# Kernel optimization log

Hardware: AMD Instinct MI355X
Metric: run time of the kernel (lower is better)

Reference implementation:

```python
import jax, jax.numpy as jnp
import numpy as np

B, T, C, H = 16, 2048, 192, 64

def setup_inputs() -> dict:
    key = jax.random.key(0)
    k1, k2, k3, k4 = jax.random.split(key, 4)
    x = jax.random.normal(k1, (B, T, C), dtype=jnp.float32)
    Wq = jax.random.normal(k2, (C, H), dtype=jnp.float32) * (C ** -0.5)
    Wk = jax.random.normal(k3, (C, H), dtype=jnp.float32) * (C ** -0.5)
    Wv = jax.random.normal(k4, (C, H), dtype=jnp.float32) * (C ** -0.5)
    return {"x": x, "Wq": Wq, "Wk": Wk, "Wv": Wv}

def reference(x, Wq, Wk, Wv):
    # One head of causal self-attention (dropout in eval mode / identity).
    q = x @ Wq                       # [B, T, H]
    k = x @ Wk                       # [B, T, H]
    v = x @ Wv                       # [B, T, H]
    scale = q.shape[-1] ** -0.5
    wei = jnp.einsum('bth,bsh->bts', q, k) * scale   # [B, T, T]
    t = wei.shape[-1]
    causal = jnp.tril(jnp.ones((t, t), dtype=bool))  # tril mask
    wei = jnp.where(causal, wei, -jnp.inf)
    wei = jax.nn.softmax(wei, axis=-1)
    out = jnp.einsum('bts,bsh->bth', wei, v)         # [B, T, H]
    return out
```

## Files before the change

### kernel.cpp

```cpp
#include <hip/hip_runtime.h>

#define B 16
#define T 2048
#define C 192
#define H 64

typedef __bf16 bf16x8 __attribute__((ext_vector_type(8)));
typedef __bf16 bf16x4 __attribute__((ext_vector_type(4)));
typedef float  f32x4  __attribute__((ext_vector_type(4)));

#define MFMA(a, b, c) __builtin_amdgcn_mfma_f32_16x16x32_bf16(a, b, c, 0, 0, 0)

#define SM_BIAS 24.0f

__global__ __launch_bounds__(512) void qkv_mfma_kernel(
    const float* __restrict__ x,
    const float* __restrict__ Wq, const float* __restrict__ Wk,
    const float* __restrict__ Wv,
    __bf16* __restrict__ qb, __bf16* __restrict__ kb, __bf16* __restrict__ vt)
{
    __shared__ __bf16 Ws[192][200];
    __shared__ __bf16 tile[128][72];

    const int tid  = threadIdx.x;
    const int w    = tid >> 6;
    const int lid  = tid & 15;
    const int quad = (tid & 63) >> 4;
    const int m0   = blockIdx.x * 128 + w * 16;

    #pragma unroll
    for (int i = 0; i < 18; i++) {
        const int p = i * 512 + tid;
        const int m = p / 3072;
        const int r = p - m * 3072;
        const int k = r >> 4;
        const int nc4 = (r & 15) << 2;
        const float* W = (m == 0) ? Wq : (m == 1) ? Wk : Wv;
        const float4 v = *(const float4*)(W + k * H + nc4);
        const int n = m * 64 + nc4;
        Ws[n + 0][k] = (__bf16)v.x;
        Ws[n + 1][k] = (__bf16)v.y;
        Ws[n + 2][k] = (__bf16)v.z;
        Ws[n + 3][k] = (__bf16)v.w;
    }

    const float* xrow = x + (size_t)(m0 + lid) * C + quad * 8;
    bf16x8 af[6];
    #pragma unroll
    for (int kc = 0; kc < 6; kc++) {
        const float4 a0 = *(const float4*)(xrow + kc * 32);
        const float4 a1 = *(const float4*)(xrow + kc * 32 + 4);
        af[kc][0] = (__bf16)a0.x; af[kc][1] = (__bf16)a0.y;
        af[kc][2] = (__bf16)a0.z; af[kc][3] = (__bf16)a0.w;
        af[kc][4] = (__bf16)a1.x; af[kc][5] = (__bf16)a1.y;
        af[kc][6] = (__bf16)a1.z; af[kc][7] = (__bf16)a1.w;
    }
    __syncthreads();

    f32x4 acc[12] = {};
    #pragma unroll
    for (int kc = 0; kc < 6; kc++)
        #pragma unroll
        for (int nt = 0; nt < 12; nt++) {
            const bf16x8 bfr =
                *(const bf16x8*)&Ws[nt * 16 + lid][kc * 32 + quad * 8];
            acc[nt] = MFMA(af[kc], bfr, acc[nt]);
        }

    #pragma unroll
    for (int nt = 0; nt < 8; nt++) {
        const int n = nt * 16 + lid;
        __bf16* dst = (n < 64) ? qb : kb;
        const int col = n & 63;
        const float scale = (n < 64) ? 0.1803368801111204f : 1.0f;
        #pragma unroll
        for (int r = 0; r < 4; r++) {
            const int row = m0 + quad * 4 + r;
            dst[(size_t)row * H + col] = (__bf16)(acc[nt][r] * scale);
        }
    }

    #pragma unroll
    for (int nt = 8; nt < 12; nt++) {
        const int col = (nt - 8) * 16 + lid;
        #pragma unroll
        for (int r = 0; r < 4; r++)
            tile[w * 16 + quad * 4 + r][col] = (__bf16)(acc[nt][r]);
    }
    __syncthreads();

    const int bb = blockIdx.x >> 4;
    const int t0 = (blockIdx.x & 15) << 7;
    #pragma unroll
    for (int it = 0; it < 2; ++it) {
        const int q   = it * 512 + tid;
        const int h   = q >> 4;
        const int tl0 = (q & 15) * 8;
        bf16x8 d;
        #pragma unroll
        for (int j = 0; j < 8; j++) d[j] = tile[tl0 + j][h];
        *(bf16x8*)(vt + ((size_t)(bb * H + h)) * T + t0 + tl0) = d;
    }
}

__global__ __launch_bounds__(512, 2) void attn_kernel(
    const __bf16* __restrict__ qb,
    const __bf16* __restrict__ kb,
    const __bf16* __restrict__ vt,
    float* __restrict__ out)
{
    __shared__ __bf16 Kb[2][2][64][72];
    __shared__ __bf16 Vb[2][2][64][68];

    const int tid  = threadIdx.x;
    const int wv   = tid >> 6;
    const int grp  = wv >> 2;
    const int w    = wv & 3;
    const int lid  = tid & 15;
    const int quad = (tid & 63) >> 4;

    const int b   = blockIdx.x & 15;
    const int pr  = blockIdx.x >> 4;
    const int qtH = 31 - pr, qtL = pr;
    const int nchH = qtH + 1;
    const int ntot = 33;
    const size_t bbase = (size_t)b * T;

    const int qH = (qtH << 6) + w * 16;
    const int qL = (qtL << 6) + w * 16;

    const __bf16* qrH = qb + (bbase + qH + lid) * H + quad * 8;
    const bf16x8 qfH0 = *(const bf16x8*)(qrH);
    const bf16x8 qfH1 = *(const bf16x8*)(qrH + 32);
    const __bf16* qrL = qb + (bbase + qL + lid) * H + quad * 8;
    const bf16x8 qfL0 = *(const bf16x8*)(qrL);
    const bf16x8 qfL1 = *(const bf16x8*)(qrL + 32);

    const __bf16* kgb = kb + bbase * H;
    const __bf16* vgb = vt + (size_t)b * H * T;

    const int ra = tid >> 3, ca = (tid & 7) * 8;

    auto keyof = [&](int i) {
        if (i > ntot - 1) i = ntot - 1;
        return (i < nchH ? i : i - nchH) << 6;
    };

    bf16x8 kr[2], vr2[2];
    auto prefetch = [&](int s) {
        #pragma unroll
        for (int g = 0; g < 2; g++) {
            const int key0 = keyof(2 * s + g);
            kr[g]  = *(const bf16x8*)(kgb + (size_t)(key0 + ra) * H + ca);
            vr2[g] = *(const bf16x8*)(vgb + (size_t)ra * T + key0 + ca);
        }
    };

    f32x4 OH[4] = {}, OL[4] = {};
    float lsH = 0.f, lsL = 0.f;

    auto doChunk = [&](f32x4 (&O)[4], float& ls, bf16x8 cq0, bf16x8 cq1,
                       int cqw, int key0, int cur) {
        const __bf16 (*Kc)[72] = Kb[cur][grp];
        const __bf16 (*Vc)[68] = Vb[cur][grp];
        bf16x8 kf[8];
        #pragma unroll
        for (int j = 0; j < 4; j++) {
            kf[2*j]   = *(const bf16x8*)&Kc[j * 16 + lid][quad * 8];
            kf[2*j+1] = *(const bf16x8*)&Kc[j * 16 + lid][32 + quad * 8];
        }
        bf16x8 bv0[4], bv1[4];
        #pragma unroll
        for (int ht = 0; ht < 4; ht++) {
            const __bf16* vr_ = &Vc[ht * 16 + lid][quad * 4];
            ((bf16x4*)&bv0[ht])[0] = *(const bf16x4*)(vr_);
            ((bf16x4*)&bv0[ht])[1] = *(const bf16x4*)(vr_ + 16);
            ((bf16x4*)&bv1[ht])[0] = *(const bf16x4*)(vr_ + 32);
            ((bf16x4*)&bv1[ht])[1] = *(const bf16x4*)(vr_ + 48);
        }
        bf16x8 af0, af1;
        const bool boundary = (key0 + 63 > cqw);
        #pragma unroll
        for (int j = 0; j < 4; j++) {
            f32x4 sS = {-SM_BIAS, -SM_BIAS, -SM_BIAS, -SM_BIAS};
            sS = MFMA(kf[2*j], cq0, sS);
            sS = MFMA(kf[2*j+1], cq1, sS);
            if (boundary) {
                #pragma unroll
                for (int r = 0; r < 4; r++)
                    if (key0 + j * 16 + quad * 4 + r > cqw + lid) sS[r] = -1e30f;
            }
            #pragma unroll
            for (int r = 0; r < 4; r++) {
                const float p = __builtin_amdgcn_exp2f(sS[r]);
                ls += p;
                if      (j == 0) af0[r]     = (__bf16)p;
                else if (j == 1) af0[4 + r] = (__bf16)p;
                else if (j == 2) af1[r]     = (__bf16)p;
                else             af1[4 + r] = (__bf16)p;
            }
        }
        #pragma unroll
        for (int ht = 0; ht < 4; ht++) {
            O[ht] = MFMA(af0, bv0[ht], O[ht]);
            O[ht] = MFMA(af1, bv1[ht], O[ht]);
        }
    };

    prefetch(0);
    int cur = 0;
    for (int s = 0; s < 17; s++) {
        *(bf16x8*)&Kb[cur][0][ra][ca] = kr[0];
        *(bf16x8*)&Kb[cur][1][ra][ca] = kr[1];
        *(bf16x8*)&Vb[cur][0][ra][ca] = vr2[0];
        *(bf16x8*)&Vb[cur][1][ra][ca] = vr2[1];
        __syncthreads();
        if (s + 1 < 17) prefetch(s + 1);

        const int i = 2 * s + grp;
        if (i < ntot) {
            const bool heavy = (i < nchH);
            const int key0 = (heavy ? i : i - nchH) << 6;
            if (heavy) doChunk(OH, lsH, qfH0, qfH1, qH, key0, cur);
            else       doChunk(OL, lsL, qfL0, qfL1, qL, key0, cur);
        }
        cur ^= 1;
    }

    __syncthreads();
    float* sO = (float*)&Kb[0][0][0][0];
    float* sL = (float*)&Vb[0][0][0][0];

    float lh = lsH; lh += __shfl_xor(lh, 16, 64); lh += __shfl_xor(lh, 32, 64);
    float ll = lsL; ll += __shfl_xor(ll, 16, 64); ll += __shfl_xor(ll, 32, 64);

    if (grp == 1) {
        #pragma unroll
        for (int ht = 0; ht < 4; ht++)
            #pragma unroll
            for (int r = 0; r < 4; r++) {
                sO[((0 * 4 + w) * 16 + quad * 4 + r) * 64 + ht * 16 + lid] = OH[ht][r];
                sO[((1 * 4 + w) * 16 + quad * 4 + r) * 64 + ht * 16 + lid] = OL[ht][r];
            }
        if ((tid & 63) < 16) {
            sL[(0 * 4 + w) * 16 + lid] = lh;
            sL[(1 * 4 + w) * 16 + lid] = ll;
        }
    }
    __syncthreads();
    if (grp == 0) {
        lh += sL[(0 * 4 + w) * 16 + lid];
        ll += sL[(1 * 4 + w) * 16 + lid];
        #pragma unroll
        for (int ht = 0; ht < 4; ht++)
            #pragma unroll
            for (int r = 0; r < 4; r++) {
                const float LrH = __shfl(lh, quad * 4 + r, 16);
                const float vH = OH[ht][r]
                    + sO[((0 * 4 + w) * 16 + quad * 4 + r) * 64 + ht * 16 + lid];
                out[(bbase + qH + quad * 4 + r) * H + ht * 16 + lid] = vH / LrH;

                const float LrL = __shfl(ll, quad * 4 + r, 16);
                const float vL = OL[ht][r]
                    + sO[((1 * 4 + w) * 16 + quad * 4 + r) * 64 + ht * 16 + lid];
                out[(bbase + qL + quad * 4 + r) * H + ht * 16 + lid] = vL / LrL;
            }
    }
}

extern "C" void kernel_launch(void* const* d_in, const int* in_sizes, int n_in,
                              void* d_out, int out_size, void* d_ws, size_t ws_size,
                              hipStream_t stream)
{
    const float* x  = (const float*)d_in[0];
    const float* Wq = (const float*)d_in[1];
    const float* Wk = (const float*)d_in[2];
    const float* Wv = (const float*)d_in[3];

    const size_t BTH = (size_t)B * T * H;
    __bf16* qbuf = (__bf16*)d_ws;
    __bf16* kbuf = qbuf + BTH;
    __bf16* vtb  = kbuf + BTH;
    float* outp = (float*)d_out;

    qkv_mfma_kernel<<<B * T / 128, 512, 0, stream>>>(x, Wq, Wk, Wv,
                                                     qbuf, kbuf, vtb);
    attn_kernel<<<B * T / 128, 512, 0, stream>>>(qbuf, kbuf, vtb, outp);
}
```

Before: 105.2 us.

## Load K/V directly from global in attention, split QKV projection across more waves

The attention kernel drops the shared-memory double-buffered K/V staging and block-wide barriers. Each 4-wave group now handles one query tile alone, loading K fragments straight from global memory with register double-buffering and V fragments per chunk. This removes the cross-group LDS reduction at the end. The QKV projection kernel doubles its block to 1024 threads, with each half computing 6 of the 12 output tiles, to cut per-wave accumulator pressure. The cost is redundant global/L2 traffic for K/V across waves, which loses the reuse the shared tiles gave, plus possible occupancy limits from the 1024-thread launch bounds.

```diff
diff --git a/kernel.cpp b/kernel.cpp
--- a/kernel.cpp
+++ b/kernel.cpp
@@ -13,7 +13,7 @@
 
 #define SM_BIAS 24.0f
 
-__global__ __launch_bounds__(512) void qkv_mfma_kernel(
+__global__ __launch_bounds__(1024, 4) void qkv_mfma_kernel(
     const float* __restrict__ x,
     const float* __restrict__ Wq, const float* __restrict__ Wk,
     const float* __restrict__ Wv,
@@ -23,14 +23,16 @@
     __shared__ __bf16 tile[128][72];
 
     const int tid  = threadIdx.x;
-    const int w    = tid >> 6;
+    const int wv   = tid >> 6;
+    const int w8   = wv & 7;
+    const int ng   = wv >> 3;
     const int lid  = tid & 15;
     const int quad = (tid & 63) >> 4;
-    const int m0   = blockIdx.x * 128 + w * 16;
-
-    #pragma unroll
-    for (int i = 0; i < 18; i++) {
-        const int p = i * 512 + tid;
+    const int m0   = blockIdx.x * 128 + w8 * 16;
+
+    #pragma unroll
+    for (int i = 0; i < 9; i++) {
+        const int p = i * 1024 + tid;
         const int m = p / 3072;
         const int r = p - m * 3072;
         const int k = r >> 4;
@@ -57,43 +59,43 @@
     }
     __syncthreads();
 
-    f32x4 acc[12] = {};
+    f32x4 acc[6] = {};
     #pragma unroll
     for (int kc = 0; kc < 6; kc++)
         #pragma unroll
-        for (int nt = 0; nt < 12; nt++) {
+        for (int nt = 0; nt < 6; nt++) {
+            const int ntg = ng * 6 + nt;
             const bf16x8 bfr =
-                *(const bf16x8*)&Ws[nt * 16 + lid][kc * 32 + quad * 8];
+                *(const bf16x8*)&Ws[ntg * 16 + lid][kc * 32 + quad * 8];
             acc[nt] = MFMA(af[kc], bfr, acc[nt]);
         }
 
     #pragma unroll
-    for (int nt = 0; nt < 8; nt++) {
-        const int n = nt * 16 + lid;
-        __bf16* dst = (n < 64) ? qb : kb;
-        const int col = n & 63;
-        const float scale = (n < 64) ? 0.1803368801111204f : 1.0f;
-        #pragma unroll
-        for (int r = 0; r < 4; r++) {
-            const int row = m0 + quad * 4 + r;
-            dst[(size_t)row * H + col] = (__bf16)(acc[nt][r] * scale);
-        }
-    }
-
-    #pragma unroll
-    for (int nt = 8; nt < 12; nt++) {
-        const int col = (nt - 8) * 16 + lid;
-        #pragma unroll
-        for (int r = 0; r < 4; r++)
-            tile[w * 16 + quad * 4 + r][col] = (__bf16)(acc[nt][r]);
+    for (int nt = 0; nt < 6; nt++) {
+        const int ntg = ng * 6 + nt;
+        const int n = ntg * 16 + lid;
+        if (ntg < 8) {
+            __bf16* dst = (n < 64) ? qb : kb;
+            const int col = n & 63;
+            const float scale = (n < 64) ? 0.1803368801111204f : 1.0f;
+            #pragma unroll
+            for (int r = 0; r < 4; r++) {
+                const int row = m0 + quad * 4 + r;
+                dst[(size_t)row * H + col] = (__bf16)(acc[nt][r] * scale);
+            }
+        } else {
+            const int col = n - 128;
+            #pragma unroll
+            for (int r = 0; r < 4; r++)
+                tile[w8 * 16 + quad * 4 + r][col] = (__bf16)(acc[nt][r]);
+        }
     }
     __syncthreads();
 
     const int bb = blockIdx.x >> 4;
     const int t0 = (blockIdx.x & 15) << 7;
-    #pragma unroll
-    for (int it = 0; it < 2; ++it) {
-        const int q   = it * 512 + tid;
+    {
+        const int q   = tid;
         const int h   = q >> 4;
         const int tl0 = (q & 15) * 8;
         bf16x8 d;
@@ -109,9 +111,6 @@
     const __bf16* __restrict__ vt,
     float* __restrict__ out)
 {
-    __shared__ __bf16 Kb[2][2][64][72];
-    __shared__ __bf16 Vb[2][2][64][68];
-
     const int tid  = threadIdx.x;
     const int wv   = tid >> 6;
     const int grp  = wv >> 2;
@@ -121,74 +120,61 @@
 
     const int b   = blockIdx.x & 15;
     const int pr  = blockIdx.x >> 4;
-    const int qtH = 31 - pr, qtL = pr;
-    const int nchH = qtH + 1;
-    const int ntot = 33;
+    const int qt  = grp ? pr : (31 - pr);
+    const int nch = qt + 1;
     const size_t bbase = (size_t)b * T;
-
-    const int qH = (qtH << 6) + w * 16;
-    const int qL = (qtL << 6) + w * 16;
-
-    const __bf16* qrH = qb + (bbase + qH + lid) * H + quad * 8;
-    const bf16x8 qfH0 = *(const bf16x8*)(qrH);
-    const bf16x8 qfH1 = *(const bf16x8*)(qrH + 32);
-    const __bf16* qrL = qb + (bbase + qL + lid) * H + quad * 8;
-    const bf16x8 qfL0 = *(const bf16x8*)(qrL);
-    const bf16x8 qfL1 = *(const bf16x8*)(qrL + 32);
+    const int qX  = (qt << 6) + w * 16;
+
+    const __bf16* qr = qb + (bbase + qX + lid) * H + quad * 8;
+    const bf16x8 qf0 = *(const bf16x8*)(qr);
+    const bf16x8 qf1 = *(const bf16x8*)(qr + 32);
 
     const __bf16* kgb = kb + bbase * H;
     const __bf16* vgb = vt + (size_t)b * H * T;
 
-    const int ra = tid >> 3, ca = (tid & 7) * 8;
-
-    auto keyof = [&](int i) {
-        if (i > ntot - 1) i = ntot - 1;
-        return (i < nchH ? i : i - nchH) << 6;
+    f32x4 O[4] = {};
+    float ls = 0.f;
+
+    bf16x8 kfA[8], kfB[8];
+
+    auto loadK = [&](bf16x8 (&kf)[8], int key0) {
+        #pragma unroll
+        for (int j = 0; j < 4; j++) {
+            const __bf16* kp =
+                kgb + (size_t)(key0 + j * 16 + lid) * H + quad * 8;
+            kf[2 * j]     = *(const bf16x8*)(kp);
+            kf[2 * j + 1] = *(const bf16x8*)(kp + 32);
+        }
     };
 
-    bf16x8 kr[2], vr2[2];
-    auto prefetch = [&](int s) {
-        #pragma unroll
-        for (int g = 0; g < 2; g++) {
-            const int key0 = keyof(2 * s + g);
-            kr[g]  = *(const bf16x8*)(kgb + (size_t)(key0 + ra) * H + ca);
-            vr2[g] = *(const bf16x8*)(vgb + (size_t)ra * T + key0 + ca);
-        }
-    };
-
-    f32x4 OH[4] = {}, OL[4] = {};
-    float lsH = 0.f, lsL = 0.f;
-
-    auto doChunk = [&](f32x4 (&O)[4], float& ls, bf16x8 cq0, bf16x8 cq1,
-                       int cqw, int key0, int cur) {
-        const __bf16 (*Kc)[72] = Kb[cur][grp];
-        const __bf16 (*Vc)[68] = Vb[cur][grp];
-        bf16x8 kf[8];
-        #pragma unroll
-        for (int j = 0; j < 4; j++) {
-            kf[2*j]   = *(const bf16x8*)&Kc[j * 16 + lid][quad * 8];
-            kf[2*j+1] = *(const bf16x8*)&Kc[j * 16 + lid][32 + quad * 8];
-        }
+    auto chunk = [&](bf16x8 (&kf)[8], bf16x8 (&kfn)[8], int i) {
+        if (i >= nch) return;
+        const int key0 = i << 6;
+
         bf16x8 bv0[4], bv1[4];
         #pragma unroll
         for (int ht = 0; ht < 4; ht++) {
-            const __bf16* vr_ = &Vc[ht * 16 + lid][quad * 4];
-            ((bf16x4*)&bv0[ht])[0] = *(const bf16x4*)(vr_);
-            ((bf16x4*)&bv0[ht])[1] = *(const bf16x4*)(vr_ + 16);
-            ((bf16x4*)&bv1[ht])[0] = *(const bf16x4*)(vr_ + 32);
-            ((bf16x4*)&bv1[ht])[1] = *(const bf16x4*)(vr_ + 48);
-        }
+            const __bf16* vp =
+                vgb + (size_t)(ht * 16 + lid) * T + key0 + quad * 4;
+            ((bf16x4*)&bv0[ht])[0] = *(const bf16x4*)(vp);
+            ((bf16x4*)&bv0[ht])[1] = *(const bf16x4*)(vp + 16);
+            ((bf16x4*)&bv1[ht])[0] = *(const bf16x4*)(vp + 32);
+            ((bf16x4*)&bv1[ht])[1] = *(const bf16x4*)(vp + 48);
+        }
+        if (i + 1 < nch) loadK(kfn, (i + 1) << 6);
+
+        const bool boundary = (key0 + 63 > qX);
         bf16x8 af0, af1;
-        const bool boundary = (key0 + 63 > cqw);
         #pragma unroll
         for (int j = 0; j < 4; j++) {
             f32x4 sS = {-SM_BIAS, -SM_BIAS, -SM_BIAS, -SM_BIAS};
-            sS = MFMA(kf[2*j], cq0, sS);
-            sS = MFMA(kf[2*j+1], cq1, sS);
+            sS = MFMA(kf[2 * j], qf0, sS);
+            sS = MFMA(kf[2 * j + 1], qf1, sS);
             if (boundary) {
                 #pragma unroll
                 for (int r = 0; r < 4; r++)
-                    if (key0 + j * 16 + quad * 4 + r > cqw + lid) sS[r] = -1e30f;
+                    if (key0 + j * 16 + quad * 4 + r > qX + lid)
+                        sS[r] = -1e30f;
             }
             #pragma unroll
             for (int r = 0; r < 4; r++) {
@@ -207,65 +193,23 @@
         }
     };
 
-    prefetch(0);
-    int cur = 0;
-    for (int s = 0; s < 17; s++) {
-        *(bf16x8*)&Kb[cur][0][ra][ca] = kr[0];
-        *(bf16x8*)&Kb[cur][1][ra][ca] = kr[1];
-        *(bf16x8*)&Vb[cur][0][ra][ca] = vr2[0];
-        *(bf16x8*)&Vb[cur][1][ra][ca] = vr2[1];
-        __syncthreads();
-        if (s + 1 < 17) prefetch(s + 1);
-
-        const int i = 2 * s + grp;
-        if (i < ntot) {
-            const bool heavy = (i < nchH);
-            const int key0 = (heavy ? i : i - nchH) << 6;
-            if (heavy) doChunk(OH, lsH, qfH0, qfH1, qH, key0, cur);
-            else       doChunk(OL, lsL, qfL0, qfL1, qL, key0, cur);
-        }
-        cur ^= 1;
-    }
-
-    __syncthreads();
-    float* sO = (float*)&Kb[0][0][0][0];
-    float* sL = (float*)&Vb[0][0][0][0];
-
-    float lh = lsH; lh += __shfl_xor(lh, 16, 64); lh += __shfl_xor(lh, 32, 64);
-    float ll = lsL; ll += __shfl_xor(ll, 16, 64); ll += __shfl_xor(ll, 32, 64);
-
-    if (grp == 1) {
-        #pragma unroll
-        for (int ht = 0; ht < 4; ht++)
-            #pragma unroll
-            for (int r = 0; r < 4; r++) {
-                sO[((0 * 4 + w) * 16 + quad * 4 + r) * 64 + ht * 16 + lid] = OH[ht][r];
-                sO[((1 * 4 + w) * 16 + quad * 4 + r) * 64 + ht * 16 + lid] = OL[ht][r];
-            }
-        if ((tid & 63) < 16) {
-            sL[(0 * 4 + w) * 16 + lid] = lh;
-            sL[(1 * 4 + w) * 16 + lid] = ll;
-        }
-    }
-    __syncthreads();
-    if (grp == 0) {
-        lh += sL[(0 * 4 + w) * 16 + lid];
-        ll += sL[(1 * 4 + w) * 16 + lid];
-        #pragma unroll
-        for (int ht = 0; ht < 4; ht++)
-            #pragma unroll
-            for (int r = 0; r < 4; r++) {
-                const float LrH = __shfl(lh, quad * 4 + r, 16);
-                const float vH = OH[ht][r]
-                    + sO[((0 * 4 + w) * 16 + quad * 4 + r) * 64 + ht * 16 + lid];
-                out[(bbase + qH + quad * 4 + r) * H + ht * 16 + lid] = vH / LrH;
-
-                const float LrL = __shfl(ll, quad * 4 + r, 16);
-                const float vL = OL[ht][r]
-                    + sO[((1 * 4 + w) * 16 + quad * 4 + r) * 64 + ht * 16 + lid];
-                out[(bbase + qL + quad * 4 + r) * H + ht * 16 + lid] = vL / LrL;
-            }
-    }
+    loadK(kfA, 0);
+    for (int i = 0; i < nch; i += 2) {
+        chunk(kfA, kfB, i);
+        chunk(kfB, kfA, i + 1);
+    }
+
+    float l = ls;
+    l += __shfl_xor(l, 16, 64);
+    l += __shfl_xor(l, 32, 64);
+    #pragma unroll
+    for (int ht = 0; ht < 4; ht++)
+        #pragma unroll
+        for (int r = 0; r < 4; r++) {
+            const float Lr = __shfl(l, quad * 4 + r, 16);
+            out[(bbase + qX + quad * 4 + r) * H + ht * 16 + lid] =
+                O[ht][r] / Lr;
+        }
 }
 
 extern "C" void kernel_launch(void* const* d_in, const int* in_sizes, int n_in,
@@ -283,7 +227,7 @@
     __bf16* vtb  = kbuf + BTH;
     float* outp = (float*)d_out;
 
-    qkv_mfma_kernel<<<B * T / 128, 512, 0, stream>>>(x, Wq, Wk, Wv,
-                                                     qbuf, kbuf, vtb);
+    qkv_mfma_kernel<<<B * T / 128, 1024, 0, stream>>>(x, Wq, Wk, Wv,
+                                                      qbuf, kbuf, vtb);
     attn_kernel<<<B * T / 128, 512, 0, stream>>>(qbuf, kbuf, vtb, outp);
 }
```

After: 173.3 us. 64.8% more time.

## Split paired heavy/light query tiles into separate blocks with doubled grid

Applied to the files above, without the earlier changes.

Each attention block used to process a heavy and a light 64-row query tile together, always running 17 steps. Now each block handles a single query tile, running a variable number of steps that depends on its causal extent, and the grid is doubled to 512 blocks. Heavy tiles are scheduled first (the first half of the grid) to help load balance. Launch bounds are raised to 4 blocks per CU to allow more occupancy from fewer live registers. The cost is that balanced pairing within a block is lost, so the outcome depends on the hardware block scheduler, and each block re-reads K/V on its own.

```diff
diff --git a/kernel.cpp b/kernel.cpp
--- a/kernel.cpp
+++ b/kernel.cpp
@@ -103,7 +103,7 @@
     }
 }
 
-__global__ __launch_bounds__(512, 2) void attn_kernel(
+__global__ __launch_bounds__(512, 4) void attn_kernel(
     const __bf16* __restrict__ qb,
     const __bf16* __restrict__ kb,
     const __bf16* __restrict__ vt,
@@ -119,22 +119,20 @@
     const int lid  = tid & 15;
     const int quad = (tid & 63) >> 4;
 
-    const int b   = blockIdx.x & 15;
-    const int pr  = blockIdx.x >> 4;
-    const int qtH = 31 - pr, qtL = pr;
-    const int nchH = qtH + 1;
-    const int ntot = 33;
+    const int half = blockIdx.x >> 8;
+    const int rem  = blockIdx.x & 255;
+    const int b    = rem & 15;
+    const int pr   = rem >> 4;
+    const int qt   = half ? pr : (31 - pr);
+    const int nch  = qt + 1;
+    const int nsteps = (nch + 1) >> 1;
     const size_t bbase = (size_t)b * T;
 
-    const int qH = (qtH << 6) + w * 16;
-    const int qL = (qtL << 6) + w * 16;
-
-    const __bf16* qrH = qb + (bbase + qH + lid) * H + quad * 8;
-    const bf16x8 qfH0 = *(const bf16x8*)(qrH);
-    const bf16x8 qfH1 = *(const bf16x8*)(qrH + 32);
-    const __bf16* qrL = qb + (bbase + qL + lid) * H + quad * 8;
-    const bf16x8 qfL0 = *(const bf16x8*)(qrL);
-    const bf16x8 qfL1 = *(const bf16x8*)(qrL + 32);
+    const int qX = (qt << 6) + w * 16;
+
+    const __bf16* qr = qb + (bbase + qX + lid) * H + quad * 8;
+    const bf16x8 qf0 = *(const bf16x8*)(qr);
+    const bf16x8 qf1 = *(const bf16x8*)(qr + 32);
 
     const __bf16* kgb = kb + bbase * H;
     const __bf16* vgb = vt + (size_t)b * H * T;
@@ -142,8 +140,8 @@
     const int ra = tid >> 3, ca = (tid & 7) * 8;
 
     auto keyof = [&](int i) {
-        if (i > ntot - 1) i = ntot - 1;
-        return (i < nchH ? i : i - nchH) << 6;
+        if (i > nch - 1) i = nch - 1;
+        return i << 6;
     };
 
     bf16x8 kr[2], vr2[2];
@@ -156,11 +154,10 @@
         }
     };
 
-    f32x4 OH[4] = {}, OL[4] = {};
-    float lsH = 0.f, lsL = 0.f;
-
-    auto doChunk = [&](f32x4 (&O)[4], float& ls, bf16x8 cq0, bf16x8 cq1,
-                       int cqw, int key0, int cur) {
+    f32x4 O[4] = {};
+    float ls = 0.f;
+
+    auto doChunk = [&](int key0, int cur) {
         const __bf16 (*Kc)[72] = Kb[cur][grp];
         const __bf16 (*Vc)[68] = Vb[cur][grp];
         bf16x8 kf[8];
@@ -179,16 +176,16 @@
             ((bf16x4*)&bv1[ht])[1] = *(const bf16x4*)(vr_ + 48);
         }
         bf16x8 af0, af1;
-        const bool boundary = (key0 + 63 > cqw);
+        const bool boundary = (key0 + 63 > qX);
         #pragma unroll
         for (int j = 0; j < 4; j++) {
             f32x4 sS = {-SM_BIAS, -SM_BIAS, -SM_BIAS, -SM_BIAS};
-            sS = MFMA(kf[2*j], cq0, sS);
-            sS = MFMA(kf[2*j+1], cq1, sS);
+            sS = MFMA(kf[2*j], qf0, sS);
+            sS = MFMA(kf[2*j+1], qf1, sS);
             if (boundary) {
                 #pragma unroll
                 for (int r = 0; r < 4; r++)
-                    if (key0 + j * 16 + quad * 4 + r > cqw + lid) sS[r] = -1e30f;
+                    if (key0 + j * 16 + quad * 4 + r > qX + lid) sS[r] = -1e30f;
             }
             #pragma unroll
             for (int r = 0; r < 4; r++) {
@@ -209,21 +206,16 @@
 
     prefetch(0);
     int cur = 0;
-    for (int s = 0; s < 17; s++) {
+    for (int s = 0; s < nsteps; s++) {
         *(bf16x8*)&Kb[cur][0][ra][ca] = kr[0];
         *(bf16x8*)&Kb[cur][1][ra][ca] = kr[1];
         *(bf16x8*)&Vb[cur][0][ra][ca] = vr2[0];
         *(bf16x8*)&Vb[cur][1][ra][ca] = vr2[1];
         __syncthreads();
-        if (s + 1 < 17) prefetch(s + 1);
+        if (s + 1 < nsteps) prefetch(s + 1);
 
         const int i = 2 * s + grp;
-        if (i < ntot) {
-            const bool heavy = (i < nchH);
-            const int key0 = (heavy ? i : i - nchH) << 6;
-            if (heavy) doChunk(OH, lsH, qfH0, qfH1, qH, key0, cur);
-            else       doChunk(OL, lsL, qfL0, qfL1, qL, key0, cur);
-        }
+        if (i < nch) doChunk(i << 6, cur);
         cur ^= 1;
     }
 
@@ -231,39 +223,29 @@
     float* sO = (float*)&Kb[0][0][0][0];
     float* sL = (float*)&Vb[0][0][0][0];
 
-    float lh = lsH; lh += __shfl_xor(lh, 16, 64); lh += __shfl_xor(lh, 32, 64);
-    float ll = lsL; ll += __shfl_xor(ll, 16, 64); ll += __shfl_xor(ll, 32, 64);
+    float l = ls;
+    l += __shfl_xor(l, 16, 64);
+    l += __shfl_xor(l, 32, 64);
 
     if (grp == 1) {
+        #pragma unroll
+        for (int ht = 0; ht < 4; ht++)
+            #pragma unroll
+            for (int r = 0; r < 4; r++)
+                sO[(w * 16 + quad * 4 + r) * 64 + ht * 16 + lid] = O[ht][r];
+        if ((tid & 63) < 16) sL[w * 16 + lid] = l;
+    }
+    __syncthreads();
+    if (grp == 0) {
+        l += sL[w * 16 + lid];
         #pragma unroll
         for (int ht = 0; ht < 4; ht++)
             #pragma unroll
             for (int r = 0; r < 4; r++) {
-                sO[((0 * 4 + w) * 16 + quad * 4 + r) * 64 + ht * 16 + lid] = OH[ht][r];
-                sO[((1 * 4 + w) * 16 + quad * 4 + r) * 64 + ht * 16 + lid] = OL[ht][r];
-            }
-        if ((tid & 63) < 16) {
-            sL[(0 * 4 + w) * 16 + lid] = lh;
-            sL[(1 * 4 + w) * 16 + lid] = ll;
-        }
-    }
-    __syncthreads();
-    if (grp == 0) {
-        lh += sL[(0 * 4 + w) * 16 + lid];
-        ll += sL[(1 * 4 + w) * 16 + lid];
-        #pragma unroll
-        for (int ht = 0; ht < 4; ht++)
-            #pragma unroll
-            for (int r = 0; r < 4; r++) {
-                const float LrH = __shfl(lh, quad * 4 + r, 16);
-                const float vH = OH[ht][r]
-                    + sO[((0 * 4 + w) * 16 + quad * 4 + r) * 64 + ht * 16 + lid];
-                out[(bbase + qH + quad * 4 + r) * H + ht * 16 + lid] = vH / LrH;
-
-                const float LrL = __shfl(ll, quad * 4 + r, 16);
-                const float vL = OL[ht][r]
-                    + sO[((1 * 4 + w) * 16 + quad * 4 + r) * 64 + ht * 16 + lid];
-                out[(bbase + qL + quad * 4 + r) * H + ht * 16 + lid] = vL / LrL;
+                const float Lr = __shfl(l, quad * 4 + r, 16);
+                const float v = O[ht][r]
+                    + sO[(w * 16 + quad * 4 + r) * 64 + ht * 16 + lid];
+                out[(bbase + qX + quad * 4 + r) * H + ht * 16 + lid] = v / Lr;
             }
     }
 }
@@ -285,5 +267,5 @@
 
     qkv_mfma_kernel<<<B * T / 128, 512, 0, stream>>>(x, Wq, Wk, Wv,
                                                      qbuf, kbuf, vtb);
-    attn_kernel<<<B * T / 128, 512, 0, stream>>>(qbuf, kbuf, vtb, outp);
+    attn_kernel<<<B * T / 128 * 2, 512, 0, stream>>>(qbuf, kbuf, vtb, outp);
 }
```

After: 101.6 us. -3.4%, faster.

## Fuse QKV projection and attention into one cooperative kernel with grid sync

Applied to the files above, without the earlier changes.

Replaces the two-kernel QKV+attention pipeline with a small weight pre-transpose kernel plus a single cooperative kernel. Each block projects exactly the query rows it later attends over, synchronises the whole grid, then runs the unchanged attention loop. Weights are pre-packed in MFMA fragment order so each block loads them with plain vector copies instead of a scattered transpose into shared memory. This saves one kernel launch gap and the per-block weight transpose, but adds an extra small launch and a grid-wide barrier, and needs all 256 blocks to be co-resident.

```diff
diff --git a/kernel.cpp b/kernel.cpp
--- a/kernel.cpp
+++ b/kernel.cpp
@@ -1,4 +1,7 @@
 #include <hip/hip_runtime.h>
+#include <hip/hip_cooperative_groups.h>
+
+namespace cg = cooperative_groups;
 
 #define B 16
 #define T 2048
@@ -13,258 +16,272 @@
 
 #define SM_BIAS 24.0f
 
-__global__ __launch_bounds__(512) void qkv_mfma_kernel(
+__global__ __launch_bounds__(512) void wtrans_kernel(
+    const float* __restrict__ Wq, const float* __restrict__ Wk,
+    const float* __restrict__ Wv, __bf16* __restrict__ Wf)
+{
+    const int idx  = blockIdx.x * 512 + threadIdx.x;
+    const int ntg  = idx / 384;
+    const int rem  = idx - ntg * 384;
+    const int kc   = rem >> 6;
+    const int lane = rem & 63;
+    const float* Wm = (ntg < 4) ? Wq : (ntg < 8) ? Wk : Wv;
+    const int nl = ((ntg & 3) << 4) + (lane & 15);
+    const int k0 = kc * 32 + (lane >> 4) * 8;
+    bf16x8 d;
+    #pragma unroll
+    for (int j = 0; j < 8; j++) d[j] = (__bf16)Wm[(k0 + j) * H + nl];
+    *(bf16x8*)(Wf + (size_t)idx * 8) = d;
+}
+
+__global__ __launch_bounds__(512) void fused_kernel(
     const float* __restrict__ x,
-    const float* __restrict__ Wq, const float* __restrict__ Wk,
-    const float* __restrict__ Wv,
-    __bf16* __restrict__ qb, __bf16* __restrict__ kb, __bf16* __restrict__ vt)
+    const __bf16* __restrict__ Wf,
+    __bf16* __restrict__ qb, __bf16* __restrict__ kb, __bf16* __restrict__ vt,
+    float* __restrict__ out)
 {
-    __shared__ __bf16 Ws[192][200];
-    __shared__ __bf16 tile[128][72];
+    __shared__ __bf16 smem[46080];
 
     const int tid  = threadIdx.x;
-    const int w    = tid >> 6;
     const int lid  = tid & 15;
     const int quad = (tid & 63) >> 4;
-    const int m0   = blockIdx.x * 128 + w * 16;
-
-    #pragma unroll
-    for (int i = 0; i < 18; i++) {
-        const int p = i * 512 + tid;
-        const int m = p / 3072;
-        const int r = p - m * 3072;
-        const int k = r >> 4;
-        const int nc4 = (r & 15) << 2;
-        const float* W = (m == 0) ? Wq : (m == 1) ? Wk : Wv;
-        const float4 v = *(const float4*)(W + k * H + nc4);
-        const int n = m * 64 + nc4;
-        Ws[n + 0][k] = (__bf16)v.x;
-        Ws[n + 1][k] = (__bf16)v.y;
-        Ws[n + 2][k] = (__bf16)v.z;
-        Ws[n + 3][k] = (__bf16)v.w;
-    }
-
-    const float* xrow = x + (size_t)(m0 + lid) * C + quad * 8;
-    bf16x8 af[6];
-    #pragma unroll
-    for (int kc = 0; kc < 6; kc++) {
-        const float4 a0 = *(const float4*)(xrow + kc * 32);
-        const float4 a1 = *(const float4*)(xrow + kc * 32 + 4);
-        af[kc][0] = (__bf16)a0.x; af[kc][1] = (__bf16)a0.y;
-        af[kc][2] = (__bf16)a0.z; af[kc][3] = (__bf16)a0.w;
-        af[kc][4] = (__bf16)a1.x; af[kc][5] = (__bf16)a1.y;
-        af[kc][6] = (__bf16)a1.z; af[kc][7] = (__bf16)a1.w;
-    }
-    __syncthreads();
-
-    f32x4 acc[12] = {};
-    #pragma unroll
-    for (int kc = 0; kc < 6; kc++)
-        #pragma unroll
-        for (int nt = 0; nt < 12; nt++) {
-            const bf16x8 bfr =
-                *(const bf16x8*)&Ws[nt * 16 + lid][kc * 32 + quad * 8];
-            acc[nt] = MFMA(af[kc], bfr, acc[nt]);
-        }
-
-    #pragma unroll
-    for (int nt = 0; nt < 8; nt++) {
-        const int n = nt * 16 + lid;
-        __bf16* dst = (n < 64) ? qb : kb;
-        const int col = n & 63;
-        const float scale = (n < 64) ? 0.1803368801111204f : 1.0f;
-        #pragma unroll
-        for (int r = 0; r < 4; r++) {
-            const int row = m0 + quad * 4 + r;
-            dst[(size_t)row * H + col] = (__bf16)(acc[nt][r] * scale);
-        }
-    }
-
-    #pragma unroll
-    for (int nt = 8; nt < 12; nt++) {
-        const int col = (nt - 8) * 16 + lid;
-        #pragma unroll
-        for (int r = 0; r < 4; r++)
-            tile[w * 16 + quad * 4 + r][col] = (__bf16)(acc[nt][r]);
-    }
-    __syncthreads();
-
-    const int bb = blockIdx.x >> 4;
-    const int t0 = (blockIdx.x & 15) << 7;
-    #pragma unroll
-    for (int it = 0; it < 2; ++it) {
-        const int q   = it * 512 + tid;
-        const int h   = q >> 4;
-        const int tl0 = (q & 15) * 8;
-        bf16x8 d;
-        #pragma unroll
-        for (int j = 0; j < 8; j++) d[j] = tile[tl0 + j][h];
-        *(bf16x8*)(vt + ((size_t)(bb * H + h)) * T + t0 + tl0) = d;
-    }
-}
-
-__global__ __launch_bounds__(512, 2) void attn_kernel(
-    const __bf16* __restrict__ qb,
-    const __bf16* __restrict__ kb,
-    const __bf16* __restrict__ vt,
-    float* __restrict__ out)
-{
-    __shared__ __bf16 Kb[2][2][64][72];
-    __shared__ __bf16 Vb[2][2][64][68];
-
-    const int tid  = threadIdx.x;
-    const int wv   = tid >> 6;
-    const int grp  = wv >> 2;
-    const int w    = wv & 3;
-    const int lid  = tid & 15;
-    const int quad = (tid & 63) >> 4;
+    const int lane = tid & 63;
 
     const int b   = blockIdx.x & 15;
     const int pr  = blockIdx.x >> 4;
     const int qtH = 31 - pr, qtL = pr;
-    const int nchH = qtH + 1;
-    const int ntot = 33;
     const size_t bbase = (size_t)b * T;
 
-    const int qH = (qtH << 6) + w * 16;
-    const int qL = (qtL << 6) + w * 16;
-
-    const __bf16* qrH = qb + (bbase + qH + lid) * H + quad * 8;
-    const bf16x8 qfH0 = *(const bf16x8*)(qrH);
-    const bf16x8 qfH1 = *(const bf16x8*)(qrH + 32);
-    const __bf16* qrL = qb + (bbase + qL + lid) * H + quad * 8;
-    const bf16x8 qfL0 = *(const bf16x8*)(qrL);
-    const bf16x8 qfL1 = *(const bf16x8*)(qrL + 32);
-
-    const __bf16* kgb = kb + bbase * H;
-    const __bf16* vgb = vt + (size_t)b * H * T;
-
-    const int ra = tid >> 3, ca = (tid & 7) * 8;
-
-    auto keyof = [&](int i) {
-        if (i > ntot - 1) i = ntot - 1;
-        return (i < nchH ? i : i - nchH) << 6;
-    };
-
-    bf16x8 kr[2], vr2[2];
-    auto prefetch = [&](int s) {
+    {
+        const int w  = tid >> 6;
+        const int rowInB = (w < 4) ? qtH * 64 + w * 16
+                                   : qtL * 64 + (w - 4) * 16;
+        const size_t m0 = bbase + rowInB;
+
+        #pragma unroll
+        for (int i = 0; i < 9; i++) {
+            const int c = i * 512 + tid;
+            *(bf16x8*)(smem + (size_t)c * 8) =
+                *(const bf16x8*)(Wf + (size_t)c * 8);
+        }
+
+        const float* xrow = x + (m0 + lid) * C + quad * 8;
+        bf16x8 af[6];
+        #pragma unroll
+        for (int kc = 0; kc < 6; kc++) {
+            const float4 a0 = *(const float4*)(xrow + kc * 32);
+            const float4 a1 = *(const float4*)(xrow + kc * 32 + 4);
+            af[kc][0] = (__bf16)a0.x; af[kc][1] = (__bf16)a0.y;
+            af[kc][2] = (__bf16)a0.z; af[kc][3] = (__bf16)a0.w;
+            af[kc][4] = (__bf16)a1.x; af[kc][5] = (__bf16)a1.y;
+            af[kc][6] = (__bf16)a1.z; af[kc][7] = (__bf16)a1.w;
+        }
+        __syncthreads();
+
+        f32x4 acc[12] = {};
+        #pragma unroll
+        for (int kc = 0; kc < 6; kc++)
+            #pragma unroll
+            for (int nt = 0; nt < 12; nt++) {
+                const int f = nt * 6 + kc;
+                const bf16x8 bfr =
+                    *(const bf16x8*)(smem + ((size_t)f * 64 + lane) * 8);
+                acc[nt] = MFMA(af[kc], bfr, acc[nt]);
+            }
+
+        #pragma unroll
+        for (int nt = 0; nt < 8; nt++) {
+            const int n = nt * 16 + lid;
+            __bf16* dst = (nt < 4) ? qb : kb;
+            const int col = n & 63;
+            const float scale = (nt < 4) ? 0.1803368801111204f : 1.0f;
+            #pragma unroll
+            for (int r = 0; r < 4; r++)
+                dst[(m0 + quad * 4 + r) * H + col] =
+                    (__bf16)(acc[nt][r] * scale);
+        }
+
+        __bf16 (*tile)[72] = reinterpret_cast<__bf16(*)[72]>(smem + 36864);
+        const int lr0 = (w & 3) * 16 + (w >> 2) * 64;
+        #pragma unroll
+        for (int nt = 8; nt < 12; nt++) {
+            const int col = (nt - 8) * 16 + lid;
+            #pragma unroll
+            for (int r = 0; r < 4; r++)
+                tile[lr0 + quad * 4 + r][col] = (__bf16)(acc[nt][r]);
+        }
+        __syncthreads();
+
+        const int h   = tid >> 3;
+        const int tl0 = (tid & 7) * 8;
         #pragma unroll
         for (int g = 0; g < 2; g++) {
-            const int key0 = keyof(2 * s + g);
-            kr[g]  = *(const bf16x8*)(kgb + (size_t)(key0 + ra) * H + ca);
-            vr2[g] = *(const bf16x8*)(vgb + (size_t)ra * T + key0 + ca);
-        }
-    };
-
-    f32x4 OH[4] = {}, OL[4] = {};
-    float lsH = 0.f, lsL = 0.f;
-
-    auto doChunk = [&](f32x4 (&O)[4], float& ls, bf16x8 cq0, bf16x8 cq1,
-                       int cqw, int key0, int cur) {
-        const __bf16 (*Kc)[72] = Kb[cur][grp];
-        const __bf16 (*Vc)[68] = Vb[cur][grp];
-        bf16x8 kf[8];
-        #pragma unroll
-        for (int j = 0; j < 4; j++) {
-            kf[2*j]   = *(const bf16x8*)&Kc[j * 16 + lid][quad * 8];
-            kf[2*j+1] = *(const bf16x8*)&Kc[j * 16 + lid][32 + quad * 8];
-        }
-        bf16x8 bv0[4], bv1[4];
-        #pragma unroll
-        for (int ht = 0; ht < 4; ht++) {
-            const __bf16* vr_ = &Vc[ht * 16 + lid][quad * 4];
-            ((bf16x4*)&bv0[ht])[0] = *(const bf16x4*)(vr_);
-            ((bf16x4*)&bv0[ht])[1] = *(const bf16x4*)(vr_ + 16);
-            ((bf16x4*)&bv1[ht])[0] = *(const bf16x4*)(vr_ + 32);
-            ((bf16x4*)&bv1[ht])[1] = *(const bf16x4*)(vr_ + 48);
-        }
-        bf16x8 af0, af1;
-        const bool boundary = (key0 + 63 > cqw);
-        #pragma unroll
-        for (int j = 0; j < 4; j++) {
-            f32x4 sS = {-SM_BIAS, -SM_BIAS, -SM_BIAS, -SM_BIAS};
-            sS = MFMA(kf[2*j], cq0, sS);
-            sS = MFMA(kf[2*j+1], cq1, sS);
-            if (boundary) {
+            const int tb = (g ? qtL : qtH) * 64;
+            bf16x8 d;
+            #pragma unroll
+            for (int j = 0; j < 8; j++) d[j] = tile[g * 64 + tl0 + j][h];
+            *(bf16x8*)(vt + ((size_t)(b * H + h)) * T + tb + tl0) = d;
+        }
+    }
+
+    cg::this_grid().sync();
+
+    {
+        const int wv   = tid >> 6;
+        const int grp  = wv >> 2;
+        const int w    = wv & 3;
+
+        const int nchH = qtH + 1;
+        const int ntot = 33;
+
+        const int qH = (qtH << 6) + w * 16;
+        const int qL = (qtL << 6) + w * 16;
+
+        auto KbP = [&](int cur, int g) {
+            return reinterpret_cast<__bf16(*)[72]>(smem + (cur * 2 + g) * 64 * 72);
+        };
+        auto VbP = [&](int cur, int g) {
+            return reinterpret_cast<__bf16(*)[68]>(smem + 18432 + (cur * 2 + g) * 64 * 68);
+        };
+
+        const __bf16* qrH = qb + (bbase + qH + lid) * H + quad * 8;
+        const bf16x8 qfH0 = *(const bf16x8*)(qrH);
+        const bf16x8 qfH1 = *(const bf16x8*)(qrH + 32);
+        const __bf16* qrL = qb + (bbase + qL + lid) * H + quad * 8;
+        const bf16x8 qfL0 = *(const bf16x8*)(qrL);
+        const bf16x8 qfL1 = *(const bf16x8*)(qrL + 32);
+
+        const __bf16* kgb = kb + bbase * H;
+        const __bf16* vgb = vt + (size_t)b * H * T;
+
+        const int ra = tid >> 3, ca = (tid & 7) * 8;
+
+        auto keyof = [&](int i) {
+            if (i > ntot - 1) i = ntot - 1;
+            return (i < nchH ? i : i - nchH) << 6;
+        };
+
+        bf16x8 kr[2], vr2[2];
+        auto prefetch = [&](int s) {
+            #pragma unroll
+            for (int g = 0; g < 2; g++) {
+                const int key0 = keyof(2 * s + g);
+                kr[g]  = *(const bf16x8*)(kgb + (size_t)(key0 + ra) * H + ca);
+                vr2[g] = *(const bf16x8*)(vgb + (size_t)ra * T + key0 + ca);
+            }
+        };
+
+        f32x4 OH[4] = {}, OL[4] = {};
+        float lsH = 0.f, lsL = 0.f;
+
+        auto doChunk = [&](f32x4 (&O)[4], float& ls, bf16x8 cq0, bf16x8 cq1,
+                           int cqw, int key0, int cur) {
+            const __bf16 (*Kc)[72] = KbP(cur, grp);
+            const __bf16 (*Vc)[68] = VbP(cur, grp);
+            bf16x8 kf[8];
+            #pragma unroll
+            for (int j = 0; j < 4; j++) {
+                kf[2*j]   = *(const bf16x8*)&Kc[j * 16 + lid][quad * 8];
+                kf[2*j+1] = *(const bf16x8*)&Kc[j * 16 + lid][32 + quad * 8];
+            }
+            bf16x8 bv0[4], bv1[4];
+            #pragma unroll
+            for (int ht = 0; ht < 4; ht++) {
+                const __bf16* vr_ = &Vc[ht * 16 + lid][quad * 4];
+                ((bf16x4*)&bv0[ht])[0] = *(const bf16x4*)(vr_);
+                ((bf16x4*)&bv0[ht])[1] = *(const bf16x4*)(vr_ + 16);
+                ((bf16x4*)&bv1[ht])[0] = *(const bf16x4*)(vr_ + 32);
+                ((bf16x4*)&bv1[ht])[1] = *(const bf16x4*)(vr_ + 48);
+            }
+            bf16x8 af0, af1;
+            const bool boundary = (key0 + 63 > cqw);
+            #pragma unroll
+            for (int j = 0; j < 4; j++) {
+                f32x4 sS = {-SM_BIAS, -SM_BIAS, -SM_BIAS, -SM_BIAS};
+                sS = MFMA(kf[2*j], cq0, sS);
+                sS = MFMA(kf[2*j+1], cq1, sS);
+                if (boundary) {
+                    #pragma unroll
+                    for (int r = 0; r < 4; r++)
+                        if (key0 + j * 16 + quad * 4 + r > cqw + lid)
+                            sS[r] = -1e30f;
+                }
                 #pragma unroll
-                for (int r = 0; r < 4; r++)
-                    if (key0 + j * 16 + quad * 4 + r > cqw + lid) sS[r] = -1e30f;
-            }
-            #pragma unroll
-            for (int r = 0; r < 4; r++) {
-                const float p = __builtin_amdgcn_exp2f(sS[r]);
-                ls += p;
-                if      (j == 0) af0[r]     = (__bf16)p;
-                else if (j == 1) af0[4 + r] = (__bf16)p;
-                else if (j == 2) af1[r]     = (__bf16)p;
-                else             af1[4 + r] = (__bf16)p;
-            }
-        }
-        #pragma unroll
-        for (int ht = 0; ht < 4; ht++) {
-            O[ht] = MFMA(af0, bv0[ht], O[ht]);
-            O[ht] = MFMA(af1, bv1[ht], O[ht]);
-        }
-    };
-
-    prefetch(0);
-    int cur = 0;
-    for (int s = 0; s < 17; s++) {
-        *(bf16x8*)&Kb[cur][0][ra][ca] = kr[0];
-        *(bf16x8*)&Kb[cur][1][ra][ca] = kr[1];
-        *(bf16x8*)&Vb[cur][0][ra][ca] = vr2[0];
-        *(bf16x8*)&Vb[cur][1][ra][ca] = vr2[1];
+                for (int r = 0; r < 4; r++) {
+                    const float p = __builtin_amdgcn_exp2f(sS[r]);
+                    ls += p;
+                    if      (j == 0) af0[r]     = (__bf16)p;
+                    else if (j == 1) af0[4 + r] = (__bf16)p;
+                    else if (j == 2) af1[r]     = (__bf16)p;
+                    else             af1[4 + r] = (__bf16)p;
+                }
+            }
+            #pragma unroll
+            for (int ht = 0; ht < 4; ht++) {
+                O[ht] = MFMA(af0, bv0[ht], O[ht]);
+                O[ht] = MFMA(af1, bv1[ht], O[ht]);
+            }
+        };
+
+        prefetch(0);
+        int cur = 0;
+        for (int s = 0; s < 17; s++) {
+            *(bf16x8*)&KbP(cur, 0)[ra][ca] = kr[0];
+            *(bf16x8*)&KbP(cur, 1)[ra][ca] = kr[1];
+            *(bf16x8*)&VbP(cur, 0)[ra][ca] = vr2[0];
+            *(bf16x8*)&VbP(cur, 1)[ra][ca] = vr2[1];
+            __syncthreads();
+            if (s + 1 < 17) prefetch(s + 1);
+
+            const int i = 2 * s + grp;
+            if (i < ntot) {
+                const bool heavy = (i < nchH);
+                const int key0 = (heavy ? i : i - nchH) << 6;
+                if (heavy) doChunk(OH, lsH, qfH0, qfH1, qH, key0, cur);
+                else       doChunk(OL, lsL, qfL0, qfL1, qL, key0, cur);
+            }
+            cur ^= 1;
+        }
+
         __syncthreads();
-        if (s + 1 < 17) prefetch(s + 1);
-
-        const int i = 2 * s + grp;
-        if (i < ntot) {
-            const bool heavy = (i < nchH);
-            const int key0 = (heavy ? i : i - nchH) << 6;
-            if (heavy) doChunk(OH, lsH, qfH0, qfH1, qH, key0, cur);
-            else       doChunk(OL, lsL, qfL0, qfL1, qL, key0, cur);
-        }
-        cur ^= 1;
-    }
-
-    __syncthreads();
-    float* sO = (float*)&Kb[0][0][0][0];
-    float* sL = (float*)&Vb[0][0][0][0];
-
-    float lh = lsH; lh += __shfl_xor(lh, 16, 64); lh += __shfl_xor(lh, 32, 64);
-    float ll = lsL; ll += __shfl_xor(ll, 16, 64); ll += __shfl_xor(ll, 32, 64);
-
-    if (grp == 1) {
-        #pragma unroll
-        for (int ht = 0; ht < 4; ht++)
-            #pragma unroll
-            for (int r = 0; r < 4; r++) {
-                sO[((0 * 4 + w) * 16 + quad * 4 + r) * 64 + ht * 16 + lid] = OH[ht][r];
-                sO[((1 * 4 + w) * 16 + quad * 4 + r) * 64 + ht * 16 + lid] = OL[ht][r];
-            }
-        if ((tid & 63) < 16) {
-            sL[(0 * 4 + w) * 16 + lid] = lh;
-            sL[(1 * 4 + w) * 16 + lid] = ll;
-        }
-    }
-    __syncthreads();
-    if (grp == 0) {
-        lh += sL[(0 * 4 + w) * 16 + lid];
-        ll += sL[(1 * 4 + w) * 16 + lid];
-        #pragma unroll
-        for (int ht = 0; ht < 4; ht++)
-            #pragma unroll
-            for (int r = 0; r < 4; r++) {
-                const float LrH = __shfl(lh, quad * 4 + r, 16);
-                const float vH = OH[ht][r]
-                    + sO[((0 * 4 + w) * 16 + quad * 4 + r) * 64 + ht * 16 + lid];
-                out[(bbase + qH + quad * 4 + r) * H + ht * 16 + lid] = vH / LrH;
-
-                const float LrL = __shfl(ll, quad * 4 + r, 16);
-                const float vL = OL[ht][r]
-                    + sO[((1 * 4 + w) * 16 + quad * 4 + r) * 64 + ht * 16 + lid];
-                out[(bbase + qL + quad * 4 + r) * H + ht * 16 + lid] = vL / LrL;
-            }
+        float* sO = (float*)smem;
+        float* sL = (float*)(smem + 18432);
+
+        float lh = lsH; lh += __shfl_xor(lh, 16, 64); lh += __shfl_xor(lh, 32, 64);
+        float ll = lsL; ll += __shfl_xor(ll, 16, 64); ll += __shfl_xor(ll, 32, 64);
+
+        if (grp == 1) {
+            #pragma unroll
+            for (int ht = 0; ht < 4; ht++)
+                #pragma unroll
+                for (int r = 0; r < 4; r++) {
+                    sO[((0 * 4 + w) * 16 + quad * 4 + r) * 64 + ht * 16 + lid] = OH[ht][r];
+                    sO[((1 * 4 + w) * 16 + quad * 4 + r) * 64 + ht * 16 + lid] = OL[ht][r];
+                }
+            if ((tid & 63) < 16) {
+                sL[(0 * 4 + w) * 16 + lid] = lh;
+                sL[(1 * 4 + w) * 16 + lid] = ll;
+            }
+        }
+        __syncthreads();
+        if (grp == 0) {
+            lh += sL[(0 * 4 + w) * 16 + lid];
+            ll += sL[(1 * 4 + w) * 16 + lid];
+            #pragma unroll
+            for (int ht = 0; ht < 4; ht++)
+                #pragma unroll
+                for (int r = 0; r < 4; r++) {
+                    const float LrH = __shfl(lh, quad * 4 + r, 16);
+                    const float vH = OH[ht][r]
+                        + sO[((0 * 4 + w) * 16 + quad * 4 + r) * 64 + ht * 16 + lid];
+                    out[(bbase + qH + quad * 4 + r) * H + ht * 16 + lid] = vH / LrH;
+
+                    const float LrL = __shfl(ll, quad * 4 + r, 16);
+                    const float vL = OL[ht][r]
+                        + sO[((1 * 4 + w) * 16 + quad * 4 + r) * 64 + ht * 16 + lid];
+                    out[(bbase + qL + quad * 4 + r) * H + ht * 16 + lid] = vL / LrL;
+                }
+        }
     }
 }
 
@@ -281,9 +298,13 @@
     __bf16* qbuf = (__bf16*)d_ws;
     __bf16* kbuf = qbuf + BTH;
     __bf16* vtb  = kbuf + BTH;
+    __bf16* Wfb  = vtb + BTH;
     float* outp = (float*)d_out;
 
-    qkv_mfma_kernel<<<B * T / 128, 512, 0, stream>>>(x, Wq, Wk, Wv,
-                                                     qbuf, kbuf, vtb);
-    attn_kernel<<<B * T / 128, 512, 0, stream>>>(qbuf, kbuf, vtb, outp);
+    wtrans_kernel<<<9, 512, 0, stream>>>(Wq, Wk, Wv, Wfb);
+
+    void* args[] = {(void*)&x, (void*)&Wfb, (void*)&qbuf, (void*)&kbuf,
+                    (void*)&vtb, (void*)&outp};
+    hipLaunchCooperativeKernel((const void*)fused_kernel, dim3(256), dim3(512),
+                               args, 0, stream);
 }
```

After: 148.2 us. 1.41x slower.
